# Optimization experiments

Hardware: AMD Instinct MI355X
Metric: run time of the kernel (lower is better)

## Reference

```python
import jax, jax.numpy as jnp
import numpy as np

N_NODES = 10000
N_EDGES = 640000
HID = 128


def setup_inputs() -> dict:
    key = jax.random.key(0)
    ks = jax.random.split(key, 8)
    h = jax.random.normal(ks[0], (N_NODES, HID), dtype=jnp.float32)
    edge_index = jax.random.randint(ks[1], (2, N_EDGES), 0, N_NODES, dtype=jnp.int64)
    edge_attr = jax.random.normal(ks[2], (N_EDGES, 1), dtype=jnp.float32)
    s1 = 1.0 / np.sqrt(2 * HID + 1)
    s2 = 1.0 / np.sqrt(HID)
    s3 = 1.0 / np.sqrt(2 * HID)
    return {
        "h": h,
        "edge_index": edge_index,
        "edge_attr": edge_attr,
        "msg_w1": jax.random.normal(ks[3], (2 * HID + 1, HID), dtype=jnp.float32) * s1,
        "msg_b1": jnp.zeros((HID,), dtype=jnp.float32),
        "msg_w2": jax.random.normal(ks[4], (HID, HID), dtype=jnp.float32) * s2,
        "msg_b2": jnp.zeros((HID,), dtype=jnp.float32),
        "upd_w1": jax.random.normal(ks[5], (2 * HID, HID), dtype=jnp.float32) * s3,
        "upd_b1": jnp.zeros((HID,), dtype=jnp.float32),
        "upd_w2": jax.random.normal(ks[6], (HID, HID), dtype=jnp.float32) * s2,
        "upd_b2": jnp.zeros((HID,), dtype=jnp.float32),
    }


def reference(h, edge_index, edge_attr, msg_w1, msg_b1, msg_w2, msg_b2,
              upd_w1, upd_b1, upd_w2, upd_b2):
    src, dst = edge_index[0], edge_index[1]
    # gather -> concat: [E, 2*HID+1]
    m_in = jnp.concatenate([h[src], h[dst], edge_attr], axis=1)
    # message MLP
    msg = jax.nn.relu(m_in @ msg_w1 + msg_b1) @ msg_w2 + msg_b2
    # scatter-add over destination nodes: [N, HID]
    agg = jax.ops.segment_sum(msg, dst, num_segments=h.shape[0])
    # update MLP with residual
    upd_in = jnp.concatenate([h, agg], axis=1)
    upd = jax.nn.relu(upd_in @ upd_w1 + upd_b1) @ upd_w2 + upd_b2
    return h + upd
```

## Files before the change

kernel.cpp:

```cpp
#include <hip/hip_runtime.h>
#include <hip/hip_bf16.h>

#define HID 128
#define NNODES 10000
#define NEDGES 640000
#define NBIN 625
#define NPB 16
#define BINCAP 1408
#define SCATB 250
#define EPT 10
#define SLAB 2560
#define PBOT_S 256

typedef __attribute__((ext_vector_type(8))) short bf16x8;
typedef __attribute__((ext_vector_type(8))) _Float16 h8;
typedef __attribute__((ext_vector_type(2))) _Float16 h2;
typedef __attribute__((ext_vector_type(4))) float f32x4;

__device__ inline short f2bf(float f) {
  unsigned u = __builtin_bit_cast(unsigned, f);
  u = (u + 0x7fffu + ((u >> 16) & 1u)) >> 16;
  return (short)u;
}

__global__ __launch_bounds__(256) void k_partA(
    const int* __restrict__ eidxraw, const float* __restrict__ ea,
    uint2* __restrict__ part, int* __restrict__ pboT,
    const float* __restrict__ h,
    const float* __restrict__ mw1, const float* __restrict__ mw2,
    const float* __restrict__ uw1, const float* __restrict__ uw2,
    short* __restrict__ pW2, short* __restrict__ pU1, short* __restrict__ pU2,
    const float* __restrict__ b1,
    _Float16* __restrict__ Xs, _Float16* __restrict__ cvecH) {
  __shared__ int histL[NBIN + 1];
  __shared__ int offsL[NBIN + 1];
  __shared__ int spL[256];
  __shared__ __align__(16) uint2 slab[SLAB];
  const int bid = blockIdx.x;
  const int tid = threadIdx.x;

  if (bid < SCATB) {
    for (int i = tid; i < NBIN + 1; i += 256) histL[i] = 0;
    __syncthreads();
    bool is64 = true;
#pragma unroll
    for (int k = 0; k < 16; ++k) is64 = is64 && (eidxraw[2 * k + 1] == 0);
    unsigned pk[EPT];
    float av[EPT];
    const int ebase = bid * SLAB;
#pragma unroll
    for (int r = 0; r < EPT; ++r) {
      int e = ebase + r * 256 + tid;
      int sv = is64 ? eidxraw[2 * e] : eidxraw[e];
      int dv = is64 ? eidxraw[2 * (NEDGES + e)] : eidxraw[NEDGES + e];
      pk[r] = ((unsigned)dv << 16) | (unsigned)sv;
      av[r] = ea[e];
      atomicAdd(&histL[dv >> 4], 1);
    }
    __syncthreads();
    int c0 = 0, c1 = 0, c2 = 0;
    {
      int b0 = tid * 3;
      if (b0 < NBIN) c0 = histL[b0];
      if (b0 + 1 < NBIN) c1 = histL[b0 + 1];
      if (b0 + 2 < NBIN) c2 = histL[b0 + 2];
    }
    int s = c0 + c1 + c2;
    spL[tid] = s;
    __syncthreads();
    for (int d = 1; d < 256; d <<= 1) {
      int v = (tid >= d) ? spL[tid - d] : 0;
      __syncthreads();
      spL[tid] += v;
      __syncthreads();
    }
    int run = spL[tid] - s;
    {
      int b0 = tid * 3;
      if (b0 < NBIN)     { offsL[b0] = run;     histL[b0] = run;     run += c0; }
      if (b0 + 1 < NBIN) { offsL[b0 + 1] = run; histL[b0 + 1] = run; run += c1; }
      if (b0 + 2 < NBIN) { offsL[b0 + 2] = run; histL[b0 + 2] = run; }
    }
    if (tid == 255) offsL[NBIN] = spL[255];
    __syncthreads();
#pragma unroll
    for (int r = 0; r < EPT; ++r) {
      int bin = pk[r] >> 20;
      int pos = atomicAdd(&histL[bin], 1);
      slab[pos] = make_uint2(pk[r], __builtin_bit_cast(unsigned, av[r]));
    }
    __syncthreads();
    for (int i = tid; i < SLAB; i += 256) part[bid * SLAB + i] = slab[i];
    for (int i = tid; i < NBIN + 1; i += 256) pboT[i * PBOT_S + bid] = offsL[i];
  } else if (bid < 282) {
    int pb = bid - SCATB;
    const float* W; short* outp; int t;
    if (pb < 8)       { W = mw2; outp = pW2; t = pb * 256; }
    else if (pb < 24) { W = uw1; outp = pU1; t = (pb - 8) * 256; }
    else              { W = uw2; outp = pU2; t = (pb - 24) * 256; }
    t += tid;
    int ll = t & 63, nt = (t >> 6) & 7, kt = t >> 9;
    int col = nt * 16 + (ll & 15);
    int k0 = kt * 32 + ((ll >> 4) << 3);
    bf16x8 o;
#pragma unroll
    for (int j = 0; j < 8; ++j) o[j] = f2bf(W[(k0 + j) * HID + col]);
    reinterpret_cast<bf16x8*>(outp)[t] = o;
  } else {
    const int wv = tid >> 6, l = tid & 63;
    const int lr = l & 15, lg = l >> 4;
    const int rbase = (bid - 282) * 64 + wv * 16;
    int rA = rbase + lr;
    if (rA > NNODES - 1) rA = NNODES - 1;
    const float* hrow = h + (size_t)rA * HID;
    const float* W1a = mw1;
    const float* W1b = mw1 + 128 * HID;

    const f32x4 zero = {0.f, 0.f, 0.f, 0.f};
    f32x4 accA[8], accB[8];
#pragma unroll
    for (int nt = 0; nt < 8; ++nt) { accA[nt] = zero; accB[nt] = zero; }
#pragma unroll
    for (int kt = 0; kt < 4; ++kt) {
      f32x4 a0 = *reinterpret_cast<const f32x4*>(hrow + kt * 32 + lg * 8);
      f32x4 a1 = *reinterpret_cast<const f32x4*>(hrow + kt * 32 + lg * 8 + 4);
      h8 af;
#pragma unroll
      for (int j = 0; j < 4; ++j) { af[j] = (_Float16)a0[j]; af[4 + j] = (_Float16)a1[j]; }
      const int k0 = kt * 32 + lg * 8;
#pragma unroll
      for (int nt = 0; nt < 8; ++nt) {
        const int col = nt * 16 + lr;
        h8 bfa, bfb;
#pragma unroll
        for (int j = 0; j < 8; ++j) {
          bfa[j] = (_Float16)W1a[(k0 + j) * HID + col];
          bfb[j] = (_Float16)W1b[(k0 + j) * HID + col];
        }
        accA[nt] = __builtin_amdgcn_mfma_f32_16x16x32_f16(af, bfa, accA[nt], 0, 0, 0);
        accB[nt] = __builtin_amdgcn_mfma_f32_16x16x32_f16(af, bfb, accB[nt], 0, 0, 0);
      }
    }
#pragma unroll
    for (int nt = 0; nt < 8; ++nt) {
      const int col = nt * 16 + lr;
      const float bb = b1[col];
#pragma unroll
      for (int i = 0; i < 4; ++i) {
        int row = rbase + lg * 4 + i;
        if (row < NNODES) {
          Xs[row * HID + col] = (_Float16)accA[nt][i];
          cvecH[row * HID + col] = (_Float16)(accB[nt][i] + bb);
        }
      }
    }
  }
}

__global__ __launch_bounds__(256) void k_merged(
    const _Float16* __restrict__ Xs, const uint2* __restrict__ part,
    const int* __restrict__ pboT, const _Float16* __restrict__ cvecH,
    const float* __restrict__ w1raw, const float* __restrict__ hf,
    const short* __restrict__ pW2, const float* __restrict__ b2,
    const short* __restrict__ pU1, const float* __restrict__ bu1,
    const short* __restrict__ pU2, const float* __restrict__ bu2,
    float* __restrict__ out) {
  __shared__ __align__(16) uint2 eraw[BINCAP];
  __shared__ __align__(16) uint2 efin[BINCAP];
  __shared__ __align__(16) short ldsR[NPB][136];
  __shared__ int spL[256];
  __shared__ int cnt16[NPB], off16[NPB], cur16[NPB];
  short* ldsA = (short*)eraw;
  short* ldsB = (short*)efin;
  const int b = blockIdx.x;
  const int tid = threadIdx.x;
  const int wv = tid >> 6, l = tid & 63;
  const int lr = l & 15, lg = l >> 4;
  const int nb = b * NPB;

  if (tid < NPB) cnt16[tid] = 0;
  int o0 = 0, cnt_t = 0;
  if (tid < SCATB) {
    o0 = pboT[b * PBOT_S + tid];
    cnt_t = pboT[(b + 1) * PBOT_S + tid] - o0;
  }
  spL[tid] = cnt_t;
  __syncthreads();
  for (int d = 1; d < 256; d <<= 1) {
    int v = (tid >= d) ? spL[tid - d] : 0;
    __syncthreads();
    spL[tid] += v;
    __syncthreads();
  }
  const int base = spL[tid] - cnt_t;
  for (int i = 0; i < cnt_t; ++i) {
    uint2 ent = part[tid * SLAB + o0 + i];
    int pos = base + i;
    if (pos < BINCAP) {
      atomicAdd(&cnt16[(int)(ent.x >> 16) & 15], 1);
      eraw[pos] = ent;
    }
  }
  __syncthreads();
  int total = spL[255];
  if (total > BINCAP) total = BINCAP;
  if (tid < NPB) {
    int v = cnt16[tid];
    int x = v;
#pragma unroll
    for (int d = 1; d < NPB; d <<= 1) {
      int y = __shfl_up(x, d);
      if (tid >= d) x += y;
    }
    off16[tid] = x - v;
    cur16[tid] = x - v;
  }
  __syncthreads();
  for (int i = tid; i < total; i += 256) {
    uint2 ent = eraw[i];
    int local = (int)(ent.x >> 16) & 15;
    int pos = atomicAdd(&cur16[local], 1);
    efin[pos] = make_uint2(ent.x & 0xFFFFu, ent.y);
  }
  __syncthreads();

  h2 wl2[4];
  {
    f32x4 w0 = *reinterpret_cast<const f32x4*>(w1raw + 256 * HID + lr * 8);
    f32x4 w1v = *reinterpret_cast<const f32x4*>(w1raw + 256 * HID + lr * 8 + 4);
    wl2[0] = h2{(_Float16)w0[0], (_Float16)w0[1]};
    wl2[1] = h2{(_Float16)w0[2], (_Float16)w0[3]};
    wl2[2] = h2{(_Float16)w1v[0], (_Float16)w1v[1]};
    wl2[3] = h2{(_Float16)w1v[2], (_Float16)w1v[3]};
  }
  const h2 zero2 = h2{(_Float16)0.f, (_Float16)0.f};

#pragma unroll
  for (int q = 0; q < 4; ++q) {
    const int local = wv * 4 + q;
    const int node = nb + local;
    const int off = off16[local];
    const int deg = cnt16[local];
    h2 cv2[4];
    {
      h8 c = *reinterpret_cast<const h8*>(cvecH + node * HID + lr * 8);
#pragma unroll
      for (int p = 0; p < 4; ++p) cv2[p] = h2{c[2 * p], c[2 * p + 1]};
    }
    h2 s2[4] = {zero2, zero2, zero2, zero2};

    const int deg16 = deg & ~15;
    for (int j0 = 0; j0 < deg16; j0 += 16) {
      h8 xs_[4];
      h2 av2_[4];
#pragma unroll
      for (int u = 0; u < 4; ++u) {
        uint2 ent = efin[off + j0 + u * 4 + lg];
        _Float16 a = (_Float16)__builtin_bit_cast(float, ent.y);
        av2_[u] = h2{a, a};
        xs_[u] = *reinterpret_cast<const h8*>(Xs + (int)ent.x * HID + lr * 8);
      }
#pragma unroll
      for (int u = 0; u < 4; ++u) {
#pragma unroll
        for (int p = 0; p < 4; ++p) {
          h2 x2 = h2{xs_[u][2 * p], xs_[u][2 * p + 1]};
          h2 t = x2 + cv2[p] + av2_[u] * wl2[p];
          s2[p] += __builtin_elementwise_max(t, zero2);
        }
      }
    }
    if (deg16 < deg) {
      h8 xs_[4];
      h2 av2_[4];
      bool val_[4];
#pragma unroll
      for (int u = 0; u < 4; ++u) {
        int j = deg16 + u * 4 + lg;
        val_[u] = (j < deg);
        int jc = val_[u] ? j : (deg > 0 ? deg - 1 : 0);
        uint2 ent = efin[off + jc];
        _Float16 a = (_Float16)__builtin_bit_cast(float, ent.y);
        av2_[u] = h2{a, a};
        xs_[u] = *reinterpret_cast<const h8*>(Xs + (int)ent.x * HID + lr * 8);
      }
#pragma unroll
      for (int u = 0; u < 4; ++u) {
#pragma unroll
        for (int p = 0; p < 4; ++p) {
          h2 x2 = h2{xs_[u][2 * p], xs_[u][2 * p + 1]};
          h2 t = x2 + cv2[p] + av2_[u] * wl2[p];
          t = __builtin_elementwise_max(t, zero2);
          s2[p] += val_[u] ? t : zero2;
        }
      }
    }
    float acc[8];
#pragma unroll
    for (int p = 0; p < 4; ++p) {
      acc[2 * p] = (float)s2[p][0];
      acc[2 * p + 1] = (float)s2[p][1];
    }
#pragma unroll
    for (int k = 0; k < 8; ++k) {
      acc[k] += __shfl_xor(acc[k], 16);
      acc[k] += __shfl_xor(acc[k], 32);
    }
    if (l < 16) {
      bf16x8 r;
#pragma unroll
      for (int k = 0; k < 8; ++k) r[k] = f2bf(acc[k]);
      *reinterpret_cast<bf16x8*>(&ldsR[local][lr * 8]) = r;
    }
  }
  __syncthreads();

  const int nt0 = wv * 2;
  const f32x4 zero = {0.f, 0.f, 0.f, 0.f};

  f32x4 acc0[2] = {zero, zero};
#pragma unroll
  for (int kt = 0; kt < 4; ++kt) {
    bf16x8 af = *reinterpret_cast<const bf16x8*>(&ldsR[lr][kt * 32 + lg * 8]);
#pragma unroll
    for (int t = 0; t < 2; ++t) {
      bf16x8 bf = reinterpret_cast<const bf16x8*>(pW2)[(kt * 8 + nt0 + t) * 64 + l];
      acc0[t] = __builtin_amdgcn_mfma_f32_16x16x32_bf16(af, bf, acc0[t], 0, 0, 0);
    }
  }
#pragma unroll
  for (int t = 0; t < 2; ++t) {
    const int col = (nt0 + t) * 16 + lr;
    const float bb = b2[col];
#pragma unroll
    for (int i = 0; i < 4; ++i) {
      int row = lg * 4 + i;
      float degr = (float)cnt16[row];
      ldsA[row * 136 + col] = f2bf(acc0[t][i] + degr * bb);
    }
  }
  __syncthreads();

  f32x4 acc1[2] = {zero, zero};
  const float* hrow = hf + (size_t)(nb + lr) * HID;
#pragma unroll
  for (int kt = 0; kt < 8; ++kt) {
    bf16x8 af;
    if (kt < 4) {
      f32x4 a0 = *reinterpret_cast<const f32x4*>(hrow + kt * 32 + lg * 8);
      f32x4 a1 = *reinterpret_cast<const f32x4*>(hrow + kt * 32 + lg * 8 + 4);
#pragma unroll
      for (int j = 0; j < 4; ++j) { af[j] = f2bf(a0[j]); af[4 + j] = f2bf(a1[j]); }
    } else {
      af = *reinterpret_cast<const bf16x8*>(&ldsA[lr * 136 + (kt - 4) * 32 + lg * 8]);
    }
#pragma unroll
    for (int t = 0; t < 2; ++t) {
      bf16x8 bf = reinterpret_cast<const bf16x8*>(pU1)[(kt * 8 + nt0 + t) * 64 + l];
      acc1[t] = __builtin_amdgcn_mfma_f32_16x16x32_bf16(af, bf, acc1[t], 0, 0, 0);
    }
  }
#pragma unroll
  for (int t = 0; t < 2; ++t) {
    const int col = (nt0 + t) * 16 + lr;
    const float bb = bu1[col];
#pragma unroll
    for (int i = 0; i < 4; ++i)
      ldsB[(lg * 4 + i) * 136 + col] = f2bf(fmaxf(acc1[t][i] + bb, 0.f));
  }
  __syncthreads();

  f32x4 acc2[2] = {zero, zero};
#pragma unroll
  for (int kt = 0; kt < 4; ++kt) {
    bf16x8 af = *reinterpret_cast<const bf16x8*>(&ldsB[lr * 136 + kt * 32 + lg * 8]);
#pragma unroll
    for (int t = 0; t < 2; ++t) {
      bf16x8 bf = reinterpret_cast<const bf16x8*>(pU2)[(kt * 8 + nt0 + t) * 64 + l];
      acc2[t] = __builtin_amdgcn_mfma_f32_16x16x32_bf16(af, bf, acc2[t], 0, 0, 0);
    }
  }
#pragma unroll
  for (int t = 0; t < 2; ++t) {
    const int col = (nt0 + t) * 16 + lr;
    const float bb = bu2[col];
#pragma unroll
    for (int i = 0; i < 4; ++i) {
      int row = nb + lg * 4 + i;
      out[row * HID + col] = hf[row * HID + col] + acc2[t][i] + bb;
    }
  }
}

extern "C" void kernel_launch(void* const* d_in, const int* in_sizes, int n_in,
                              void* d_out, int out_size, void* d_ws, size_t ws_size,
                              hipStream_t stream) {
  const float* h    = (const float*)d_in[0];
  const int*   eidx = (const int*)d_in[1];
  const float* ea   = (const float*)d_in[2];
  const float* mw1  = (const float*)d_in[3];
  const float* mb1  = (const float*)d_in[4];
  const float* mw2  = (const float*)d_in[5];
  const float* mb2  = (const float*)d_in[6];
  const float* uw1  = (const float*)d_in[7];
  const float* ub1  = (const float*)d_in[8];
  const float* uw2  = (const float*)d_in[9];
  const float* ub2  = (const float*)d_in[10];
  float* out = (float*)d_out;

  char* ws = (char*)d_ws;
  uint2*     part  = (uint2*)(ws + 0);
  int*       pboT  = (int*)(ws + 5120000);
  _Float16*  Xs    = (_Float16*)(ws + 5761024);
  _Float16*  cvecH = (_Float16*)(ws + 8321024);
  short*     pW2   = (short*)(ws + 10881024);
  short*     pU1   = (short*)(ws + 10913792);
  short*     pU2   = (short*)(ws + 10979328);

  k_partA<<<439, 256, 0, stream>>>(eidx, ea, part, pboT, h, mw1, mw2, uw1, uw2,
                                   pW2, pU1, pU2, mb1, Xs, cvecH);
  k_merged<<<NBIN, 256, 0, stream>>>(Xs, part, pboT, cvecH, mw1, h,
                                     pW2, mb2, pU1, ub1, pU2, ub2, out);
}
```

Baseline: 58.73 us.

## Stage transposed msg_w1 in LDS, coalesce bin gather, vectorize int64 index loads

The node-projection blocks now convert msg_w1 to fp16 once per block, store it transposed in padded shared memory, and read MFMA B operands as 16-byte LDS vectors. Before, each lane issued strided scalar global loads. The bin-gather step in the merged kernel is also reorganised: eight lanes cooperate on each scatter-block segment, so reads of the partitioned edge list are coalesced, with a per-thread fallback for segments longer than 16 entries. Int64 edge indices are read as int2 loads, and the shared memory of the first kernel is unioned across roles, at the cost of a larger per-block LDS footprint.

```diff
diff --git a/kernel.cpp b/kernel.cpp
--- a/kernel.cpp
+++ b/kernel.cpp
@@ -32,14 +32,16 @@
     short* __restrict__ pW2, short* __restrict__ pU1, short* __restrict__ pU2,
     const float* __restrict__ b1,
     _Float16* __restrict__ Xs, _Float16* __restrict__ cvecH) {
-  __shared__ int histL[NBIN + 1];
-  __shared__ int offsL[NBIN + 1];
-  __shared__ int spL[256];
-  __shared__ __align__(16) uint2 slab[SLAB];
+  __shared__ __align__(16) char smemU[2 * 128 * 136 * 2];
   const int bid = blockIdx.x;
   const int tid = threadIdx.x;
 
   if (bid < SCATB) {
+    int* histL = (int*)smemU;
+    int* offsL = histL + 626;
+    int* spL   = offsL + 626;
+    uint2* slab = (uint2*)(smemU + 6048);
+
     for (int i = tid; i < NBIN + 1; i += 256) histL[i] = 0;
     __syncthreads();
     bool is64 = true;
@@ -48,11 +50,12 @@
     unsigned pk[EPT];
     float av[EPT];
     const int ebase = bid * SLAB;
+    const int2* e2 = (const int2*)eidxraw;
 #pragma unroll
     for (int r = 0; r < EPT; ++r) {
       int e = ebase + r * 256 + tid;
-      int sv = is64 ? eidxraw[2 * e] : eidxraw[e];
-      int dv = is64 ? eidxraw[2 * (NEDGES + e)] : eidxraw[NEDGES + e];
+      int sv = is64 ? e2[e].x : eidxraw[e];
+      int dv = is64 ? e2[NEDGES + e].x : eidxraw[NEDGES + e];
       pk[r] = ((unsigned)dv << 16) | (unsigned)sv;
       av[r] = ea[e];
       atomicAdd(&histL[dv >> 4], 1);
@@ -107,14 +110,29 @@
     for (int j = 0; j < 8; ++j) o[j] = f2bf(W[(k0 + j) * HID + col]);
     reinterpret_cast<bf16x8*>(outp)[t] = o;
   } else {
+    _Float16* WTa = (_Float16*)smemU;
+    _Float16* WTb = WTa + 128 * 136;
+    const float* W1a = mw1;
+    const float* W1b = mw1 + 128 * HID;
+    for (int idx = tid; idx < 128 * 32; idx += 256) {
+      int r = idx >> 5;
+      int c4 = (idx & 31) << 2;
+      f32x4 wa = *reinterpret_cast<const f32x4*>(W1a + r * HID + c4);
+      f32x4 wb = *reinterpret_cast<const f32x4*>(W1b + r * HID + c4);
+#pragma unroll
+      for (int j = 0; j < 4; ++j) {
+        WTa[(c4 + j) * 136 + r] = (_Float16)wa[j];
+        WTb[(c4 + j) * 136 + r] = (_Float16)wb[j];
+      }
+    }
+    __syncthreads();
+
     const int wv = tid >> 6, l = tid & 63;
     const int lr = l & 15, lg = l >> 4;
     const int rbase = (bid - 282) * 64 + wv * 16;
     int rA = rbase + lr;
     if (rA > NNODES - 1) rA = NNODES - 1;
     const float* hrow = h + (size_t)rA * HID;
-    const float* W1a = mw1;
-    const float* W1b = mw1 + 128 * HID;
 
     const f32x4 zero = {0.f, 0.f, 0.f, 0.f};
     f32x4 accA[8], accB[8];
@@ -131,12 +149,8 @@
 #pragma unroll
       for (int nt = 0; nt < 8; ++nt) {
         const int col = nt * 16 + lr;
-        h8 bfa, bfb;
-#pragma unroll
-        for (int j = 0; j < 8; ++j) {
-          bfa[j] = (_Float16)W1a[(k0 + j) * HID + col];
-          bfb[j] = (_Float16)W1b[(k0 + j) * HID + col];
-        }
+        h8 bfa = *reinterpret_cast<const h8*>(WTa + col * 136 + k0);
+        h8 bfb = *reinterpret_cast<const h8*>(WTb + col * 136 + k0);
         accA[nt] = __builtin_amdgcn_mfma_f32_16x16x32_f16(af, bfa, accA[nt], 0, 0, 0);
         accB[nt] = __builtin_amdgcn_mfma_f32_16x16x32_f16(af, bfb, accB[nt], 0, 0, 0);
       }
@@ -169,6 +183,7 @@
   __shared__ __align__(16) uint2 efin[BINCAP];
   __shared__ __align__(16) short ldsR[NPB][136];
   __shared__ int spL[256];
+  __shared__ int sO[256], sC[256], sB[256];
   __shared__ int cnt16[NPB], off16[NPB], cur16[NPB];
   short* ldsA = (short*)eraw;
   short* ldsB = (short*)efin;
@@ -193,12 +208,35 @@
     __syncthreads();
   }
   const int base = spL[tid] - cnt_t;
-  for (int i = 0; i < cnt_t; ++i) {
-    uint2 ent = part[tid * SLAB + o0 + i];
-    int pos = base + i;
-    if (pos < BINCAP) {
-      atomicAdd(&cnt16[(int)(ent.x >> 16) & 15], 1);
-      eraw[pos] = ent;
+  sO[tid] = o0; sC[tid] = cnt_t; sB[tid] = base;
+  __syncthreads();
+  for (int p = 0; p < 8; ++p) {
+    int s = p * 32 + wv * 8 + (l >> 3);
+    bool sok = (s < SCATB);
+    int so = sok ? sO[s] : 0;
+    int sc = sok ? sC[s] : 0;
+    int sb = sok ? sB[s] : 0;
+#pragma unroll
+    for (int r = 0; r < 2; ++r) {
+      int i = r * 8 + (l & 7);
+      if (i < sc) {
+        uint2 ent = part[s * SLAB + so + i];
+        int pos = sb + i;
+        if (pos < BINCAP) {
+          atomicAdd(&cnt16[(int)(ent.x >> 16) & 15], 1);
+          eraw[pos] = ent;
+        }
+      }
+    }
+  }
+  if (tid < SCATB && cnt_t > 16) {
+    for (int i = 16; i < cnt_t; ++i) {
+      uint2 ent = part[tid * SLAB + o0 + i];
+      int pos = base + i;
+      if (pos < BINCAP) {
+        atomicAdd(&cnt16[(int)(ent.x >> 16) & 15], 1);
+        eraw[pos] = ent;
+      }
     }
   }
   __syncthreads();
```

After: 52.40 us. 10.8% less time.
